# Kernel optimization log

Measured on AMD Instinct MI355X. Metric: run time of the kernel, lower is better.

Reference implementation:

```python
import jax, jax.numpy as jnp
import numpy as np

# ---- static configuration (from init_kwargs) ----
NY = NX = 256          # velocity model size
PML = 20               # PML width (cells) on every edge
FD_PAD = 2             # halo for 4th-order (accuracy=4) stencil
PAD = PML + FD_PAD
NYP = NY + 2 * PAD     # padded grid = 300
NXP = NX + 2 * PAD
DY = DX = 5.0          # grid spacing (m)
DT = 5e-4              # time step (s), CFL-stable for vmax=4000
NT = 250
NSHOT, NSRC, NREC = 2, 8, 64
PML_FREQ = 25.0
MAX_VEL = 4000.0

# 4th-order central FD coefficients
C1 = (1.0 / 12.0, -2.0 / 3.0, 0.0, 2.0 / 3.0, -1.0 / 12.0)   # d/dx
C2 = (-1.0 / 12.0, 4.0 / 3.0, -5.0 / 2.0, 4.0 / 3.0, -1.0 / 12.0)  # d2/dx2


def _fd(x, coefs, axis, h):
    """Central finite difference along `axis` with zero (Dirichlet) boundaries."""
    pad = [(0, 0)] * x.ndim
    pad[axis] = (2, 2)
    xp = jnp.pad(x, pad)
    n = x.shape[axis]
    out = None
    for i, c in enumerate(coefs):
        if c == 0.0:
            continue
        t = c * jax.lax.slice_in_dim(xp, i, i + n, axis=axis)
        out = t if out is None else out + t
    return out / h


def _pml_profiles(n, dx):
    """C-PML a/b profiles (Pasalic & McGarry 2010) along one padded axis."""
    i = jnp.arange(n, dtype=jnp.float32)
    lo = float(PAD)          # first interior cell
    hi = float(n - PAD - 1)  # last interior cell
    frac = jnp.clip(jnp.maximum(lo - i, i - hi) / PML, 0.0, 1.0)
    sigma_max = 3.0 * MAX_VEL * float(np.log(1000.0)) / (2.0 * PML * dx)
    sigma = sigma_max * frac ** 2
    alpha = float(np.pi) * PML_FREQ * (1.0 - frac)
    b = jnp.exp(-(sigma + alpha) * DT)
    a = sigma / (sigma + alpha + 1e-9) * (b - 1.0)
    return a.astype(jnp.float32), b.astype(jnp.float32)


def setup_inputs() -> dict:
    key = jax.random.key(0)
    k1, k2, k3, k4 = jax.random.split(key, 4)
    # realistic acoustic velocities 1500-4000 m/s
    v = 1500.0 + 2500.0 * jax.random.uniform(k1, (NY, NX), dtype=jnp.float32)
    source_amplitudes = jax.random.normal(k2, (NSHOT, NSRC, NT), dtype=jnp.float32)
    source_locations = jax.random.randint(k3, (NSHOT, NSRC, 2), 0, NY, dtype=jnp.int64)
    receiver_locations = jax.random.randint(k4, (NSHOT, NREC, 2), 0, NY, dtype=jnp.int64)
    return {
        "v": v,
        "source_amplitudes": source_amplitudes,
        "source_locations": source_locations,
        "receiver_locations": receiver_locations,
    }


def reference(v, source_amplitudes, source_locations, receiver_locations):
    # pad velocity into PML + fd halo by edge replication (per docstring)
    vp = jnp.pad(v, PAD, mode="edge")
    v2dt2 = (vp * vp) * (DT * DT)  # [NYP, NXP]

    ay, by = _pml_profiles(NYP, DY)
    ay, by = ay[:, None], by[:, None]   # broadcast over x
    ax, bx = _pml_profiles(NXP, DX)      # broadcast over y

    sy = source_locations[..., 0] + PAD   # [NSHOT, NSRC]
    sx = source_locations[..., 1] + PAD
    ry = receiver_locations[..., 0] + PAD  # [NSHOT, NREC]
    rx = receiver_locations[..., 1] + PAD
    shot_s = jnp.arange(NSHOT)[:, None]
    src_scale = v2dt2[sy, sx]  # source term is scaled by v^2*dt^2

    zeros = jnp.zeros((NSHOT, NYP, NXP), jnp.float32)
    carry0 = (zeros, zeros, zeros, zeros, zeros, zeros)

    def step(carry, amp_t):
        wfc, wfm, psiy, psix, zetay, zetax = carry
        # y direction
        dwdy = _fd(wfc, C1, -2, DY)
        d2wdy2 = _fd(wfc, C2, -2, DY * DY)
        psiy = by * psiy + ay * dwdy
        dpsiydy = _fd(psiy, C1, -2, DY)
        zetay = by * zetay + ay * (d2wdy2 + dpsiydy)
        # x direction
        dwdx = _fd(wfc, C1, -1, DX)
        d2wdx2 = _fd(wfc, C2, -1, DX * DX)
        psix = bx * psix + ax * dwdx
        dpsixdx = _fd(psix, C1, -1, DX)
        zetax = bx * zetax + ax * (d2wdx2 + dpsixdx)
        # leapfrog time update with C-PML corrections
        lap = d2wdy2 + d2wdx2 + dpsiydy + dpsixdx + zetay + zetax
        wfp = 2.0 * wfc - wfm + v2dt2 * lap
        wfp = wfp.at[shot_s, sy, sx].add(src_scale * amp_t)
        rec = wfp[shot_s, ry, rx]  # [NSHOT, NREC]
        return (wfp, wfc, psiy, psix, zetay, zetax), rec

    amps = jnp.moveaxis(source_amplitudes, -1, 0)  # [NT, NSHOT, NSRC]
    _, recs = jax.lax.scan(step, carry0, amps)
    return jnp.moveaxis(recs, 0, -1)  # [NSHOT, NREC, NT]
```

## Files before the change

kernel.cpp:

```cpp
#include <hip/hip_runtime.h>
#include <cstdint>

#define NYD   256
#define NXD   256
#define PADC  22
#define NYP_  300
#define NXP_  300
#define NTT   250
#define NSHOT_ 2
#define NSRC_  8
#define NREC_  64
#define DT_   0.0005f

#define GDN   28
#define STP   356
#define FP    (STP*STP)

#define NTX   5
#define NTY   75
#define TPS   375
#define NWG   750

__global__ void zero_kernel(float* __restrict__ p, long n) {
    long i = (long)blockIdx.x * blockDim.x + threadIdx.x;
    long stride = (long)gridDim.x * blockDim.x;
    for (; i < n; i += stride) p[i] = 0.0f;
}

__global__ void populate_kernel(const float* __restrict__ v,
                                const int* __restrict__ srcloc,
                                const int* __restrict__ recloc,
                                float* __restrict__ v2dt2,
                                float* __restrict__ prof,
                                unsigned* __restrict__ srcbin,
                                unsigned long long* __restrict__ recbin) {
    int i = blockIdx.x * 256 + threadIdx.x;

    if (i < NYP_ * NXP_) {
        int y = i / NXP_, x = i % NXP_;
        int vy = min(max(y - PADC, 0), NYD - 1);
        int vx = min(max(x - PADC, 0), NXD - 1);
        float vv = v[vy * NXD + vx];
        v2dt2[(y + GDN) * STP + (x + GDN)] = vv * vv * (DT_ * DT_);
    }

    if (i < NYP_) {
        float fi = (float)i;
        float d = fmaxf(22.0f - fi, fi - 277.0f);
        float frac = fminf(fmaxf(d * (1.0f / 20.0f), 0.0f), 1.0f);
        float sigma_max = 3.0f * 4000.0f * logf(1000.0f) / (2.0f * 20.0f * 5.0f);
        float sigma = sigma_max * frac * frac;
        float alpha = 3.14159265358979323846f * 25.0f * (1.0f - frac);
        float b = expf(-(sigma + alpha) * DT_);
        float a = sigma / (sigma + alpha + 1e-9f) * (b - 1.0f);
        prof[GDN + i] = a;
        prof[STP + GDN + i] = b;
    }

    if (i < NSHOT_ * NSRC_) {
        int sy = srcloc[2 * i] + PADC;
        int sx = srcloc[2 * i + 1] + PADC;
        int shot = i / NSRC_;
        int tl = (sy / 4) * NTX + (sx / 64);
        atomicOr(&srcbin[shot * TPS + tl], 1u << (i % NSRC_));
    }

    if (i >= 1024 && i < 1024 + NSHOT_ * NREC_) {
        int j = i - 1024;
        int ry = recloc[2 * j] + PADC;
        int rx = recloc[2 * j + 1] + PADC;
        int shot = j / NREC_;
        int tl = (ry / 4) * NTX + (rx / 64);
        atomicOr(&recbin[shot * TPS + tl], 1ull << (j % NREC_));
    }
}

__global__ __launch_bounds__(256) void step_kernel(
    const float* __restrict__ wfc_g,
    float* __restrict__ wfn_g,
    const float* __restrict__ pyr_g, float* __restrict__ pyw_g,
    const float* __restrict__ pxr_g, float* __restrict__ pxw_g,
    float* __restrict__ zy_g, float* __restrict__ zx_g,
    const float* __restrict__ v2_g, const float* __restrict__ prof,
    const unsigned* __restrict__ srcbin,
    const unsigned long long* __restrict__ recbin,
    const int* __restrict__ srcloc, const int* __restrict__ recloc,
    const float* __restrict__ amps,
    float* __restrict__ out,
    int t) {
    int orig = blockIdx.x;
    int xcd = orig & 7, idx = orig >> 3;
    int wgid = (xcd < 6) ? xcd * 94 + idx : 6 * 94 + (xcd - 6) * 93 + idx;
    int shot = wgid / TPS;
    int tl   = wgid - shot * TPS;
    int ty0  = (tl / NTX) * 4;
    int tx0  = (tl % NTX) * 64;

    const float* wfc = wfc_g + shot * FP;
    float*       wfn = wfn_g + shot * FP;
    const float* pyr = pyr_g + shot * FP;
    float*       pyw = pyw_g + shot * FP;
    const float* pxr = pxr_g + shot * FP;
    float*       pxw = pxw_g + shot * FP;
    float*       zyg = zy_g  + shot * FP;
    float*       zxg = zx_g  + shot * FP;

    __shared__ float swf[12][72];
    __shared__ float spy[8][64];
    __shared__ float spx[4][72];
    __shared__ float sya[8], syb[8], sxa[68], sxb[68];
    __shared__ int   ssy[NSRC_], ssx[NSRC_], sry[NREC_], srx[NREC_];
    __shared__ unsigned sbs;
    __shared__ unsigned long long sbr;

    const int tid = threadIdx.x;
    const int lx = tid & 63, ly = tid >> 6;
    const int y = ty0 + ly, x = tx0 + lx;
    const int g = (y + GDN) * STP + (x + GDN);

    float wm = wfn[g];
    float zy = zyg[g];
    float zx = zxg[g];
    float vd = v2_g[g];

    if (tid < 216) {
        int rr = tid / 18, cc = tid % 18;
        const float4 val = *(reinterpret_cast<const float4*>(
            wfc + (ty0 - 4 + rr + GDN) * STP + (tx0 - 4 + GDN)) + cc);
        *reinterpret_cast<float4*>(&swf[rr][cc * 4]) = val;
    }
    if (tid < 128) {
        int rr = tid / 16, cc = tid % 16;
        const float4 val = *(reinterpret_cast<const float4*>(
            pyr + (ty0 - 2 + rr + GDN) * STP + (tx0 + GDN)) + cc);
        *reinterpret_cast<float4*>(&spy[rr][cc * 4]) = val;
    }
    if (tid < 72) {
        int rr = tid / 18, cc = tid % 18;
        const float4 val = *(reinterpret_cast<const float4*>(
            pxr + (ty0 + rr + GDN) * STP + (tx0 - 4 + GDN)) + cc);
        *reinterpret_cast<float4*>(&spx[rr][cc * 4]) = val;
    }
    if (tid < 8) {
        sya[tid] = prof[GDN + ty0 - 2 + tid];
        syb[tid] = prof[STP + GDN + ty0 - 2 + tid];
        ssy[tid] = srcloc[(shot * NSRC_ + tid) * 2]     + PADC;
        ssx[tid] = srcloc[(shot * NSRC_ + tid) * 2 + 1] + PADC;
    }
    if (tid < 68) {
        sxa[tid] = prof[GDN + tx0 - 2 + tid];
        sxb[tid] = prof[STP + GDN + tx0 - 2 + tid];
    }
    if (tid < NREC_) {
        sry[tid] = recloc[(shot * NREC_ + tid) * 2]     + PADC;
        srx[tid] = recloc[(shot * NREC_ + tid) * 2 + 1] + PADC;
    }
    if (tid == 0) {
        sbs = srcbin[shot * TPS + tl];
        sbr = recbin[shot * TPS + tl];
    }
    __syncthreads();

    const float ih  = 0.2f;
    const float ih2 = 0.04f;
    const float C1A = 2.0f / 3.0f, C1B = 1.0f / 12.0f;
    const float C2A = 4.0f / 3.0f, C2B = -1.0f / 12.0f, C2C = -2.5f;

    float wy[9];
#pragma unroll
    for (int k = 0; k < 9; k++) wy[k] = swf[ly + k][lx + 4];
    float wx[9];
#pragma unroll
    for (int k = 0; k < 9; k++) wx[k] = (k == 4) ? wy[4] : swf[ly + 4][lx + k];

    float d2y = (C2B * (wy[2] + wy[6]) + C2A * (wy[3] + wy[5]) + C2C * wy[4]) * ih2;
    float d2x = (C2B * (wx[2] + wx[6]) + C2A * (wx[3] + wx[5]) + C2C * wx[4]) * ih2;

    float pny[5], pnx[5];
#pragma unroll
    for (int j = 0; j < 5; j++) {
        float dwdy = (C1A * (wy[j + 3] - wy[j + 1]) - C1B * (wy[j + 4] - wy[j])) * ih;
        pny[j] = syb[ly + j] * spy[ly + j][lx] + sya[ly + j] * dwdy;
        float dwdx = (C1A * (wx[j + 3] - wx[j + 1]) - C1B * (wx[j + 4] - wx[j])) * ih;
        pnx[j] = sxb[lx + j] * spx[ly][lx + j + 2] + sxa[lx + j] * dwdx;
    }

    float dpsiy = (C1A * (pny[3] - pny[1]) - C1B * (pny[4] - pny[0])) * ih;
    float dpsix = (C1A * (pnx[3] - pnx[1]) - C1B * (pnx[4] - pnx[0])) * ih;

    float ay_ = sya[ly + 2], by_ = syb[ly + 2];
    float ax_ = sxa[lx + 2], bx_ = sxb[lx + 2];

    zy = by_ * zy + ay_ * (d2y + dpsiy);
    zx = bx_ * zx + ax_ * (d2x + dpsix);

    float lap = d2y + d2x + dpsiy + dpsix + zy + zx;
    float wfp = 2.0f * wy[4] - wm + vd * lap;

    if (sbs) {
#pragma unroll
        for (int q = 0; q < NSRC_; q++)
            if ((sbs & (1u << q)) && ssy[q] == y && ssx[q] == x)
                wfp += vd * amps[(shot * NSRC_ + q) * NTT + t];
    }

    wfn[g] = wfp;
    pyw[g] = pny[2];
    pxw[g] = pnx[2];
    zyg[g] = zy;
    zxg[g] = zx;

    unsigned long long rb = sbr;
    while (rb) {
        int r = __ffsll(rb) - 1;
        rb &= rb - 1;
        if (sry[r] == y && srx[r] == x)
            out[(shot * NREC_ + r) * NTT + t] = wfp;
    }
}

extern "C" void kernel_launch(void* const* d_in, const int* in_sizes, int n_in,
                              void* d_out, int out_size, void* d_ws, size_t ws_size,
                              hipStream_t stream) {
    const float* v      = (const float*)d_in[0];
    const float* amps   = (const float*)d_in[1];
    const int*   srcloc = (const int*)d_in[2];
    const int*   recloc = (const int*)d_in[3];
    float* out = (float*)d_out;

    float* base = (float*)d_ws;
    float* WF0 = base;
    float* WF1 = WF0 + 2L * FP;
    float* PY0 = WF1 + 2L * FP;
    float* PY1 = PY0 + 2L * FP;
    float* PX0 = PY1 + 2L * FP;
    float* PX1 = PX0 + 2L * FP;
    float* ZY  = PX1 + 2L * FP;
    float* ZX  = ZY  + 2L * FP;
    float* V2  = ZX  + 2L * FP;
    float* PROF = V2 + FP;
    unsigned* SRCBIN = (unsigned*)(PROF + 2 * STP);
    unsigned long long* RECBIN = (unsigned long long*)(SRCBIN + NSHOT_ * TPS);

    const long total_words = 17L * FP + 2 * STP + NSHOT_ * TPS + 2L * NSHOT_ * TPS;

    zero_kernel<<<2048, 256, 0, stream>>>(base, total_words);
    populate_kernel<<<(NYP_ * NXP_ + 255) / 256, 256, 0, stream>>>(
        v, srcloc, recloc, V2, PROF, SRCBIN, RECBIN);

    for (int t = 0; t < NTT; t++) {
        const bool o = (t & 1);
        step_kernel<<<NWG, 256, 0, stream>>>(
            o ? WF1 : WF0, o ? WF0 : WF1,
            o ? PY1 : PY0, o ? PY0 : PY1,
            o ? PX1 : PX0, o ? PX0 : PX1,
            ZY, ZX, V2, PROF, SRCBIN, RECBIN,
            srcloc, recloc, amps, out, t);
    }
}
```

Measured before the change: 1.275 ms.

## Fuse two timesteps per launch with halo-expanded tiles in shared memory

Replaces the single-step kernel with a temporal-blocking kernel that advances two leapfrog steps per launch. It loads 8x32 tiles with wide halos into LDS, computes the intermediate wavefield, psi and zeta over an extended region, then finishes the second step for the interior. This halves the number of launches and the global memory round trips of wavefield and PML state. The cost is redundant halo computation, more LDS, extra ping-pong buffers, and brute-force source checks in place of source binning.

```diff
diff --git a/kernel.cpp b/kernel.cpp
--- a/kernel.cpp
+++ b/kernel.cpp
@@ -16,10 +16,12 @@
 #define STP   356
 #define FP    (STP*STP)
 
-#define NTX   5
-#define NTY   75
-#define TPS   375
-#define NWG   750
+#define BY    8
+#define BX    32
+#define NTX   10
+#define NTY   38
+#define TPS   380
+#define NWG   760
 
 __global__ void zero_kernel(float* __restrict__ p, long n) {
     long i = (long)blockIdx.x * blockDim.x + threadIdx.x;
@@ -28,11 +30,9 @@
 }
 
 __global__ void populate_kernel(const float* __restrict__ v,
-                                const int* __restrict__ srcloc,
                                 const int* __restrict__ recloc,
                                 float* __restrict__ v2dt2,
                                 float* __restrict__ prof,
-                                unsigned* __restrict__ srcbin,
                                 unsigned long long* __restrict__ recbin) {
     int i = blockIdx.x * 256 + threadIdx.x;
 
@@ -57,108 +57,114 @@
         prof[STP + GDN + i] = b;
     }
 
-    if (i < NSHOT_ * NSRC_) {
-        int sy = srcloc[2 * i] + PADC;
-        int sx = srcloc[2 * i + 1] + PADC;
-        int shot = i / NSRC_;
-        int tl = (sy / 4) * NTX + (sx / 64);
-        atomicOr(&srcbin[shot * TPS + tl], 1u << (i % NSRC_));
-    }
-
-    if (i >= 1024 && i < 1024 + NSHOT_ * NREC_) {
-        int j = i - 1024;
-        int ry = recloc[2 * j] + PADC;
-        int rx = recloc[2 * j + 1] + PADC;
-        int shot = j / NREC_;
-        int tl = (ry / 4) * NTX + (rx / 64);
-        atomicOr(&recbin[shot * TPS + tl], 1ull << (j % NREC_));
+    if (i < NSHOT_ * NREC_) {
+        int ry = recloc[2 * i] + PADC;
+        int rx = recloc[2 * i + 1] + PADC;
+        int shot = i / NREC_;
+        int tl = (ry / BY) * NTX + (rx / BX);
+        atomicOr(&recbin[shot * TPS + tl], 1ull << (i % NREC_));
     }
 }
 
-__global__ __launch_bounds__(256) void step_kernel(
+__global__ __launch_bounds__(256) void fused2_kernel(
+    const float* __restrict__ wfm_g,
     const float* __restrict__ wfc_g,
-    float* __restrict__ wfn_g,
+    float* __restrict__ w1_g,
+    float* __restrict__ w2_g,
     const float* __restrict__ pyr_g, float* __restrict__ pyw_g,
     const float* __restrict__ pxr_g, float* __restrict__ pxw_g,
-    float* __restrict__ zy_g, float* __restrict__ zx_g,
+    const float* __restrict__ zyr_g, float* __restrict__ zyw_g,
+    const float* __restrict__ zxr_g, float* __restrict__ zxw_g,
     const float* __restrict__ v2_g, const float* __restrict__ prof,
-    const unsigned* __restrict__ srcbin,
     const unsigned long long* __restrict__ recbin,
     const int* __restrict__ srcloc, const int* __restrict__ recloc,
     const float* __restrict__ amps,
     float* __restrict__ out,
     int t) {
-    int orig = blockIdx.x;
-    int xcd = orig & 7, idx = orig >> 3;
-    int wgid = (xcd < 6) ? xcd * 94 + idx : 6 * 94 + (xcd - 6) * 93 + idx;
-    int shot = wgid / TPS;
-    int tl   = wgid - shot * TPS;
-    int ty0  = (tl / NTX) * 4;
-    int tx0  = (tl % NTX) * 64;
-
+    const int orig = blockIdx.x;
+    const int wgid = (orig & 7) * 95 + (orig >> 3);
+    const int shot = wgid / TPS;
+    const int tl   = wgid - shot * TPS;
+    const int ty0  = (tl / NTX) * BY;
+    const int tx0  = (tl % NTX) * BX;
+
+    const float* wfm = wfm_g + shot * FP;
     const float* wfc = wfc_g + shot * FP;
-    float*       wfn = wfn_g + shot * FP;
+    float*       w1o = w1_g  + shot * FP;
+    float*       w2o = w2_g  + shot * FP;
     const float* pyr = pyr_g + shot * FP;
     float*       pyw = pyw_g + shot * FP;
     const float* pxr = pxr_g + shot * FP;
     float*       pxw = pxw_g + shot * FP;
-    float*       zyg = zy_g  + shot * FP;
-    float*       zxg = zx_g  + shot * FP;
-
-    __shared__ float swf[12][72];
-    __shared__ float spy[8][64];
-    __shared__ float spx[4][72];
-    __shared__ float sya[8], syb[8], sxa[68], sxb[68];
+    const float* zyr = zyr_g + shot * FP;
+    float*       zyw = zyw_g + shot * FP;
+    const float* zxr = zxr_g + shot * FP;
+    float*       zxw = zxw_g + shot * FP;
+
+    __shared__ float swf0[24][48];
+    __shared__ float spy [20][40];
+    __shared__ float spx [16][48];
+    __shared__ float swf1[16][40];
+    __shared__ float szy [16][40];
+    __shared__ float szx [16][40];
+    __shared__ float sv2 [16][40];
+    __shared__ float swm [16][40];
+    __shared__ float sya[24], syb[24], sxa[48], sxb[48];
     __shared__ int   ssy[NSRC_], ssx[NSRC_], sry[NREC_], srx[NREC_];
-    __shared__ unsigned sbs;
-    __shared__ unsigned long long sbr;
+    __shared__ unsigned long long srb;
 
     const int tid = threadIdx.x;
-    const int lx = tid & 63, ly = tid >> 6;
-    const int y = ty0 + ly, x = tx0 + lx;
-    const int g = (y + GDN) * STP + (x + GDN);
-
-    float wm = wfn[g];
-    float zy = zyg[g];
-    float zx = zxg[g];
-    float vd = v2_g[g];
-
-    if (tid < 216) {
-        int rr = tid / 18, cc = tid % 18;
-        const float4 val = *(reinterpret_cast<const float4*>(
-            wfc + (ty0 - 4 + rr + GDN) * STP + (tx0 - 4 + GDN)) + cc);
-        *reinterpret_cast<float4*>(&swf[rr][cc * 4]) = val;
-    }
-    if (tid < 128) {
-        int rr = tid / 16, cc = tid % 16;
-        const float4 val = *(reinterpret_cast<const float4*>(
-            pyr + (ty0 - 2 + rr + GDN) * STP + (tx0 + GDN)) + cc);
-        *reinterpret_cast<float4*>(&spy[rr][cc * 4]) = val;
-    }
-    if (tid < 72) {
-        int rr = tid / 18, cc = tid % 18;
-        const float4 val = *(reinterpret_cast<const float4*>(
-            pxr + (ty0 + rr + GDN) * STP + (tx0 - 4 + GDN)) + cc);
-        *reinterpret_cast<float4*>(&spx[rr][cc * 4]) = val;
-    }
-    if (tid < 8) {
-        sya[tid] = prof[GDN + ty0 - 2 + tid];
-        syb[tid] = prof[STP + GDN + ty0 - 2 + tid];
+
+#pragma unroll
+    for (int li = 0; li < 6; li++) {
+        int lin = tid + li * 256;
+        if (lin < 288) {
+            int rr = lin / 12, cc = lin % 12;
+            *reinterpret_cast<float4*>(&swf0[rr][cc * 4]) =
+                *reinterpret_cast<const float4*>(wfc + (ty0 - 8 + rr + GDN) * STP + (tx0 - 8 + GDN) + cc * 4);
+        } else if (lin < 488) {
+            int l = lin - 288; int rr = l / 10, cc = l % 10;
+            *reinterpret_cast<float4*>(&spy[rr][cc * 4]) =
+                *reinterpret_cast<const float4*>(pyr + (ty0 - 6 + rr + GDN) * STP + (tx0 - 4 + GDN) + cc * 4);
+        } else if (lin < 680) {
+            int l = lin - 488; int rr = l / 12, cc = l % 12;
+            *reinterpret_cast<float4*>(&spx[rr][cc * 4]) =
+                *reinterpret_cast<const float4*>(pxr + (ty0 - 4 + rr + GDN) * STP + (tx0 - 8 + GDN) + cc * 4);
+        } else if (lin < 840) {
+            int l = lin - 680; int rr = l / 10, cc = l % 10;
+            *reinterpret_cast<float4*>(&szy[rr][cc * 4]) =
+                *reinterpret_cast<const float4*>(zyr + (ty0 - 4 + rr + GDN) * STP + (tx0 - 4 + GDN) + cc * 4);
+        } else if (lin < 1000) {
+            int l = lin - 840; int rr = l / 10, cc = l % 10;
+            *reinterpret_cast<float4*>(&szx[rr][cc * 4]) =
+                *reinterpret_cast<const float4*>(zxr + (ty0 - 4 + rr + GDN) * STP + (tx0 - 4 + GDN) + cc * 4);
+        } else if (lin < 1160) {
+            int l = lin - 1000; int rr = l / 10, cc = l % 10;
+            *reinterpret_cast<float4*>(&sv2[rr][cc * 4]) =
+                *reinterpret_cast<const float4*>(v2_g + (ty0 - 4 + rr + GDN) * STP + (tx0 - 4 + GDN) + cc * 4);
+        } else if (lin < 1320) {
+            int l = lin - 1160; int rr = l / 10, cc = l % 10;
+            *reinterpret_cast<float4*>(&swm[rr][cc * 4]) =
+                *reinterpret_cast<const float4*>(wfm + (ty0 - 4 + rr + GDN) * STP + (tx0 - 4 + GDN) + cc * 4);
+        }
+    }
+    if (tid < 24) {
+        sya[tid] = prof[GDN + ty0 - 8 + tid];
+        syb[tid] = prof[STP + GDN + ty0 - 8 + tid];
+    }
+    if (tid < 48) {
+        sxa[tid] = prof[GDN + tx0 - 8 + tid];
+        sxb[tid] = prof[STP + GDN + tx0 - 8 + tid];
+    }
+    if (tid < NSRC_) {
         ssy[tid] = srcloc[(shot * NSRC_ + tid) * 2]     + PADC;
         ssx[tid] = srcloc[(shot * NSRC_ + tid) * 2 + 1] + PADC;
-    }
-    if (tid < 68) {
-        sxa[tid] = prof[GDN + tx0 - 2 + tid];
-        sxb[tid] = prof[STP + GDN + tx0 - 2 + tid];
     }
     if (tid < NREC_) {
         sry[tid] = recloc[(shot * NREC_ + tid) * 2]     + PADC;
         srx[tid] = recloc[(shot * NREC_ + tid) * 2 + 1] + PADC;
     }
-    if (tid == 0) {
-        sbs = srcbin[shot * TPS + tl];
-        sbr = recbin[shot * TPS + tl];
-    }
+    if (tid == 0) srb = recbin[shot * TPS + tl];
     __syncthreads();
 
     const float ih  = 0.2f;
@@ -166,56 +172,110 @@
     const float C1A = 2.0f / 3.0f, C1B = 1.0f / 12.0f;
     const float C2A = 4.0f / 3.0f, C2B = -1.0f / 12.0f, C2C = -2.5f;
 
-    float wy[9];
-#pragma unroll
-    for (int k = 0; k < 9; k++) wy[k] = swf[ly + k][lx + 4];
-    float wx[9];
-#pragma unroll
-    for (int k = 0; k < 9; k++) wx[k] = (k == 4) ? wy[4] : swf[ly + 4][lx + k];
-
-    float d2y = (C2B * (wy[2] + wy[6]) + C2A * (wy[3] + wy[5]) + C2C * wy[4]) * ih2;
-    float d2x = (C2B * (wx[2] + wx[6]) + C2A * (wx[3] + wx[5]) + C2C * wx[4]) * ih2;
-
-    float pny[5], pnx[5];
-#pragma unroll
-    for (int j = 0; j < 5; j++) {
-        float dwdy = (C1A * (wy[j + 3] - wy[j + 1]) - C1B * (wy[j + 4] - wy[j])) * ih;
-        pny[j] = syb[ly + j] * spy[ly + j][lx] + sya[ly + j] * dwdy;
-        float dwdx = (C1A * (wx[j + 3] - wx[j + 1]) - C1B * (wx[j + 4] - wx[j])) * ih;
-        pnx[j] = sxb[lx + j] * spx[ly][lx + j + 2] + sxa[lx + j] * dwdx;
-    }
-
-    float dpsiy = (C1A * (pny[3] - pny[1]) - C1B * (pny[4] - pny[0])) * ih;
-    float dpsix = (C1A * (pnx[3] - pnx[1]) - C1B * (pnx[4] - pnx[0])) * ih;
-
-    float ay_ = sya[ly + 2], by_ = syb[ly + 2];
-    float ax_ = sxa[lx + 2], bx_ = sxb[lx + 2];
-
-    zy = by_ * zy + ay_ * (d2y + dpsiy);
-    zx = bx_ * zx + ax_ * (d2x + dpsix);
-
-    float lap = d2y + d2x + dpsiy + dpsix + zy + zx;
-    float wfp = 2.0f * wy[4] - wm + vd * lap;
-
-    if (sbs) {
+#pragma unroll
+    for (int li = 0; li < 6; li++) {
+        int lin = tid + li * 256;
+        if (lin < 800) {
+            int r = lin / 40, c = lin % 40;
+            float dw = (C1A * (swf0[r + 3][c + 4] - swf0[r + 1][c + 4])
+                      - C1B * (swf0[r + 4][c + 4] - swf0[r][c + 4])) * ih;
+            spy[r][c] = syb[r + 2] * spy[r][c] + sya[r + 2] * dw;
+        } else if (lin < 1504) {
+            int l = lin - 800; int r = l / 44, c = l % 44 + 2;
+            float dw = (C1A * (swf0[r + 4][c + 1] - swf0[r + 4][c - 1])
+                      - C1B * (swf0[r + 4][c + 2] - swf0[r + 4][c - 2])) * ih;
+            spx[r][c] = sxb[c] * spx[r][c] + sxa[c] * dw;
+        }
+    }
+    __syncthreads();
+
+#pragma unroll
+    for (int li = 0; li < 3; li++) {
+        int lin = tid + li * 256;
+        if (lin < 640) {
+            int r = lin / 40, c = lin % 40;
+            float wc = swf0[r + 4][c + 4];
+            float d2y = (C2B * (swf0[r + 2][c + 4] + swf0[r + 6][c + 4])
+                       + C2A * (swf0[r + 3][c + 4] + swf0[r + 5][c + 4]) + C2C * wc) * ih2;
+            float d2x = (C2B * (swf0[r + 4][c + 2] + swf0[r + 4][c + 6])
+                       + C2A * (swf0[r + 4][c + 3] + swf0[r + 4][c + 5]) + C2C * wc) * ih2;
+            float dpy = (C1A * (spy[r + 3][c] - spy[r + 1][c])
+                       - C1B * (spy[r + 4][c] - spy[r][c])) * ih;
+            float dpx = (C1A * (spx[r][c + 5] - spx[r][c + 3])
+                       - C1B * (spx[r][c + 6] - spx[r][c + 2])) * ih;
+            float zy1 = syb[r + 4] * szy[r][c] + sya[r + 4] * (d2y + dpy);
+            float zx1 = sxb[c + 4] * szx[r][c] + sxa[c + 4] * (d2x + dpx);
+            szy[r][c] = zy1;
+            szx[r][c] = zx1;
+            float vd = sv2[r][c];
+            float w1 = 2.0f * wc - swm[r][c] + vd * (d2y + d2x + dpy + dpx + zy1 + zx1);
+            int y = ty0 - 4 + r, x = tx0 - 4 + c;
+#pragma unroll
+            for (int q = 0; q < NSRC_; q++)
+                if (ssy[q] == y && ssx[q] == x)
+                    w1 += vd * amps[(shot * NSRC_ + q) * NTT + t];
+            swf1[r][c] = w1;
+        }
+    }
+    __syncthreads();
+
+#pragma unroll
+    for (int li = 0; li < 3; li++) {
+        int lin = tid + li * 256;
+        if (lin < 384) {
+            int r = lin / 32, c = lin % 32;
+            float dw1 = (C1A * (swf1[r + 3][c + 4] - swf1[r + 1][c + 4])
+                       - C1B * (swf1[r + 4][c + 4] - swf1[r][c + 4])) * ih;
+            spy[r + 4][c + 4] = syb[r + 6] * spy[r + 4][c + 4] + sya[r + 6] * dw1;
+        } else if (lin < 672) {
+            int l = lin - 384; int r = l / 36, c2 = l % 36;
+            float dw1 = (C1A * (swf1[r + 4][c2 + 3] - swf1[r + 4][c2 + 1])
+                       - C1B * (swf1[r + 4][c2 + 4] - swf1[r + 4][c2])) * ih;
+            spx[r + 4][c2 + 6] = sxb[c2 + 6] * spx[r + 4][c2 + 6] + sxa[c2 + 6] * dw1;
+        }
+    }
+    __syncthreads();
+
+    {
+        int ly = tid >> 5, lx = tid & 31;
+        int y = ty0 + ly, x = tx0 + lx;
+        float w1c = swf1[ly + 4][lx + 4];
+        float d2y1 = (C2B * (swf1[ly + 2][lx + 4] + swf1[ly + 6][lx + 4])
+                    + C2A * (swf1[ly + 3][lx + 4] + swf1[ly + 5][lx + 4]) + C2C * w1c) * ih2;
+        float d2x1 = (C2B * (swf1[ly + 4][lx + 2] + swf1[ly + 4][lx + 6])
+                    + C2A * (swf1[ly + 4][lx + 3] + swf1[ly + 4][lx + 5]) + C2C * w1c) * ih2;
+        float dpy2 = (C1A * (spy[ly + 7][lx + 4] - spy[ly + 5][lx + 4])
+                    - C1B * (spy[ly + 8][lx + 4] - spy[ly + 4][lx + 4])) * ih;
+        float dpx2 = (C1A * (spx[ly + 4][lx + 9] - spx[ly + 4][lx + 7])
+                    - C1B * (spx[ly + 4][lx + 10] - spx[ly + 4][lx + 6])) * ih;
+        float zy2 = syb[ly + 8] * szy[ly + 4][lx + 4] + sya[ly + 8] * (d2y1 + dpy2);
+        float zx2 = sxb[lx + 8] * szx[ly + 4][lx + 4] + sxa[lx + 8] * (d2x1 + dpx2);
+        float vd = sv2[ly + 4][lx + 4];
+        float w2 = 2.0f * w1c - swf0[ly + 8][lx + 8]
+                 + vd * (d2y1 + d2x1 + dpy2 + dpx2 + zy2 + zx2);
 #pragma unroll
         for (int q = 0; q < NSRC_; q++)
-            if ((sbs & (1u << q)) && ssy[q] == y && ssx[q] == x)
-                wfp += vd * amps[(shot * NSRC_ + q) * NTT + t];
-    }
-
-    wfn[g] = wfp;
-    pyw[g] = pny[2];
-    pxw[g] = pnx[2];
-    zyg[g] = zy;
-    zxg[g] = zx;
-
-    unsigned long long rb = sbr;
-    while (rb) {
-        int r = __ffsll(rb) - 1;
-        rb &= rb - 1;
-        if (sry[r] == y && srx[r] == x)
-            out[(shot * NREC_ + r) * NTT + t] = wfp;
+            if (ssy[q] == y && ssx[q] == x)
+                w2 += vd * amps[(shot * NSRC_ + q) * NTT + t + 1];
+
+        if (y < NYP_ && x < NXP_) {
+            int g = (y + GDN) * STP + (x + GDN);
+            w1o[g] = w1c;
+            w2o[g] = w2;
+            pyw[g] = spy[ly + 6][lx + 4];
+            pxw[g] = spx[ly + 4][lx + 8];
+            zyw[g] = zy2;
+            zxw[g] = zx2;
+            unsigned long long rb = srb;
+            while (rb) {
+                int r = __ffsll(rb) - 1;
+                rb &= rb - 1;
+                if (sry[r] == y && srx[r] == x) {
+                    out[(shot * NREC_ + r) * NTT + t]     = w1c;
+                    out[(shot * NREC_ + r) * NTT + t + 1] = w2;
+                }
+            }
+        }
     }
 }
 
@@ -229,32 +289,37 @@
     float* out = (float*)d_out;
 
     float* base = (float*)d_ws;
-    float* WF0 = base;
-    float* WF1 = WF0 + 2L * FP;
-    float* PY0 = WF1 + 2L * FP;
+    float* W0  = base;
+    float* W1  = W0  + 2L * FP;
+    float* W2  = W1  + 2L * FP;
+    float* W3  = W2  + 2L * FP;
+    float* PY0 = W3  + 2L * FP;
     float* PY1 = PY0 + 2L * FP;
     float* PX0 = PY1 + 2L * FP;
     float* PX1 = PX0 + 2L * FP;
-    float* ZY  = PX1 + 2L * FP;
-    float* ZX  = ZY  + 2L * FP;
-    float* V2  = ZX  + 2L * FP;
+    float* ZY0 = PX1 + 2L * FP;
+    float* ZY1 = ZY0 + 2L * FP;
+    float* ZX0 = ZY1 + 2L * FP;
+    float* ZX1 = ZX0 + 2L * FP;
+    float* V2  = ZX1 + 2L * FP;
     float* PROF = V2 + FP;
-    unsigned* SRCBIN = (unsigned*)(PROF + 2 * STP);
-    unsigned long long* RECBIN = (unsigned long long*)(SRCBIN + NSHOT_ * TPS);
-
-    const long total_words = 17L * FP + 2 * STP + NSHOT_ * TPS + 2L * NSHOT_ * TPS;
+    unsigned long long* RECBIN = (unsigned long long*)(PROF + 2 * STP);
+
+    const long total_words = 25L * FP + 2 * STP + 2L * NSHOT_ * TPS;
 
     zero_kernel<<<2048, 256, 0, stream>>>(base, total_words);
     populate_kernel<<<(NYP_ * NXP_ + 255) / 256, 256, 0, stream>>>(
-        v, srcloc, recloc, V2, PROF, SRCBIN, RECBIN);
-
-    for (int t = 0; t < NTT; t++) {
-        const bool o = (t & 1);
-        step_kernel<<<NWG, 256, 0, stream>>>(
-            o ? WF1 : WF0, o ? WF0 : WF1,
+        v, recloc, V2, PROF, RECBIN);
+
+    for (int k = 0; k < NTT / 2; k++) {
+        const bool o = (k & 1);
+        fused2_kernel<<<NWG, 256, 0, stream>>>(
+            o ? W2 : W0, o ? W3 : W1,
+            o ? W0 : W2, o ? W1 : W3,
             o ? PY1 : PY0, o ? PY0 : PY1,
             o ? PX1 : PX0, o ? PX0 : PX1,
-            ZY, ZX, V2, PROF, SRCBIN, RECBIN,
-            srcloc, recloc, amps, out, t);
+            o ? ZY1 : ZY0, o ? ZY0 : ZY1,
+            o ? ZX1 : ZX0, o ? ZX0 : ZX1,
+            V2, PROF, RECBIN, srcloc, recloc, amps, out, 2 * k);
     }
 }
```

Result: slower. 1.315 ms (+3.1%).

## Replace per-step kernel launches with persistent cooperative kernel using neighbor flags

Applied to the files above, without the earlier changes.

Launches one cooperative persistent kernel of 190 workgroups (512 threads, 16x64 tiles) that loops over all 250 time steps. Workgroups synchronise through per-tile progress counters, waiting only on their four neighbours, and the zeta and previous-wavefield state stays in registers across steps. This removes 250 kernel launches and the per-step reload of the zeta, wfm and velocity arrays. The cost is spin-wait overhead, reliance on agent-scope relaxed atomics for ordering, and fewer workgroups in flight. The old per-step path remains as a fallback if the cooperative launch fails.

```diff
diff --git a/kernel.cpp b/kernel.cpp
--- a/kernel.cpp
+++ b/kernel.cpp
@@ -17,9 +17,22 @@
 #define FP    (STP*STP)
 
 #define NTX   5
-#define NTY   75
 #define TPS   375
 #define NWG   750
+
+#define BY2   16
+#define NTY2  19
+#define TPS2  95
+#define NWG2  190
+
+__device__ __forceinline__ unsigned long long ld_agent_u64(const float* p) {
+    return __hip_atomic_load((const unsigned long long*)p,
+                             __ATOMIC_RELAXED, __HIP_MEMORY_SCOPE_AGENT);
+}
+__device__ __forceinline__ void st_agent_f32(float* p, float v) {
+    __hip_atomic_store((unsigned*)p, __float_as_uint(v),
+                       __ATOMIC_RELAXED, __HIP_MEMORY_SCOPE_AGENT);
+}
 
 __global__ void zero_kernel(float* __restrict__ p, long n) {
     long i = (long)blockIdx.x * blockDim.x + threadIdx.x;
@@ -32,8 +45,10 @@
                                 const int* __restrict__ recloc,
                                 float* __restrict__ v2dt2,
                                 float* __restrict__ prof,
-                                unsigned* __restrict__ srcbin,
-                                unsigned long long* __restrict__ recbin) {
+                                unsigned* __restrict__ srcb4,
+                                unsigned long long* __restrict__ recb4,
+                                unsigned* __restrict__ srcb16,
+                                unsigned long long* __restrict__ recb16) {
     int i = blockIdx.x * 256 + threadIdx.x;
 
     if (i < NYP_ * NXP_) {
@@ -61,8 +76,8 @@
         int sy = srcloc[2 * i] + PADC;
         int sx = srcloc[2 * i + 1] + PADC;
         int shot = i / NSRC_;
-        int tl = (sy / 4) * NTX + (sx / 64);
-        atomicOr(&srcbin[shot * TPS + tl], 1u << (i % NSRC_));
+        atomicOr(&srcb4[shot * TPS + (sy / 4) * NTX + (sx / 64)], 1u << (i % NSRC_));
+        atomicOr(&srcb16[shot * TPS2 + (sy / BY2) * 5 + (sx / 64)], 1u << (i % NSRC_));
     }
 
     if (i >= 1024 && i < 1024 + NSHOT_ * NREC_) {
@@ -70,14 +85,170 @@
         int ry = recloc[2 * j] + PADC;
         int rx = recloc[2 * j + 1] + PADC;
         int shot = j / NREC_;
-        int tl = (ry / 4) * NTX + (rx / 64);
-        atomicOr(&recbin[shot * TPS + tl], 1ull << (j % NREC_));
+        atomicOr(&recb4[shot * TPS + (ry / 4) * NTX + (rx / 64)], 1ull << (j % NREC_));
+        atomicOr(&recb16[shot * TPS2 + (ry / BY2) * 5 + (rx / 64)], 1ull << (j % NREC_));
+    }
+}
+
+__global__ __launch_bounds__(512) void persist_kernel(
+    float* wfA, float* wfB, float* pyA, float* pyB, float* pxA, float* pxB,
+    const float* __restrict__ v2g, const float* __restrict__ profg,
+    const unsigned* __restrict__ srcb, const unsigned long long* __restrict__ recb,
+    int* prog,
+    const int* __restrict__ srcloc, const int* __restrict__ recloc,
+    const float* __restrict__ amps,
+    float* __restrict__ out) {
+    const int me   = blockIdx.x;
+    const int shot = me / TPS2;
+    const int tl   = me - shot * TPS2;
+    const int tyt  = tl / 5, txt = tl % 5;
+    const int ty0  = tyt * BY2, tx0 = txt * 64;
+
+    const int nUp = (tyt > 0)        ? me - 5 : me;
+    const int nDn = (tyt < NTY2 - 1) ? me + 5 : me;
+    const int nL  = (txt > 0)        ? me - 1 : me;
+    const int nR  = (txt < 4)        ? me + 1 : me;
+
+    __shared__ alignas(8) float swf[24][72];
+    __shared__ alignas(8) float spy[20][64];
+    __shared__ alignas(8) float spx[16][72];
+    __shared__ float sya[20], syb[20], sxa[68], sxb[68];
+    __shared__ int   ssy[NSRC_], ssx[NSRC_], sry[NREC_], srx[NREC_];
+    __shared__ unsigned sbs;
+    __shared__ unsigned long long sbr;
+
+    const int tid = threadIdx.x;
+    const int lx = tid & 63, ly = tid >> 6;
+
+    if (tid < 20) {
+        sya[tid] = profg[GDN + ty0 - 2 + tid];
+        syb[tid] = profg[STP + GDN + ty0 - 2 + tid];
+    }
+    if (tid < 68) {
+        sxa[tid] = profg[GDN + tx0 - 2 + tid];
+        sxb[tid] = profg[STP + GDN + tx0 - 2 + tid];
+    }
+    if (tid < NSRC_) {
+        ssy[tid] = srcloc[(shot * NSRC_ + tid) * 2]     + PADC;
+        ssx[tid] = srcloc[(shot * NSRC_ + tid) * 2 + 1] + PADC;
+    }
+    if (tid < NREC_) {
+        sry[tid] = recloc[(shot * NREC_ + tid) * 2]     + PADC;
+        srx[tid] = recloc[(shot * NREC_ + tid) * 2 + 1] + PADC;
+    }
+    if (tid == 0) { sbs = srcb[shot * TPS2 + tl]; sbr = recb[shot * TPS2 + tl]; }
+
+    float zyr[2] = {0.f, 0.f}, zxr[2] = {0.f, 0.f}, wmr[2] = {0.f, 0.f}, vdr[2];
+#pragma unroll
+    for (int c = 0; c < 2; ++c)
+        vdr[c] = v2g[(ty0 + ly + 8 * c + GDN) * STP + (tx0 + lx + GDN)];
+
+    const float* wfr = wfA + shot * FP;  float* wfw = wfB + shot * FP;
+    const float* pyr = pyA + shot * FP;  float* pyw = pyB + shot * FP;
+    const float* pxr = pxA + shot * FP;  float* pxw = pxB + shot * FP;
+
+    __syncthreads();
+
+    const float ih  = 0.2f;
+    const float ih2 = 0.04f;
+    const float C1A = 2.0f / 3.0f, C1B = 1.0f / 12.0f;
+    const float C2A = 4.0f / 3.0f, C2B = -1.0f / 12.0f, C2C = -2.5f;
+
+#pragma unroll 1
+    for (int it = 0; it < NTT; ++it) {
+        if (tid < 4) {
+            const int nb = (tid == 0) ? nUp : (tid == 1) ? nDn : (tid == 2) ? nL : nR;
+            while (__hip_atomic_load(&prog[nb], __ATOMIC_RELAXED, __HIP_MEMORY_SCOPE_AGENT) < it)
+                __builtin_amdgcn_s_sleep(1);
+        }
+        __syncthreads();
+
+#pragma unroll
+        for (int li = 0; li < 5; ++li) {
+            int lin = tid + li * 512;
+            if (lin < 864) {
+                int rr = lin / 36, cc = lin % 36;
+                *(unsigned long long*)&swf[rr][cc * 2] =
+                    ld_agent_u64(wfr + (ty0 - 4 + rr + GDN) * STP + (tx0 - 4 + GDN) + cc * 2);
+            } else if (lin < 1504) {
+                int l = lin - 864, rr = l / 32, cc = l % 32;
+                *(unsigned long long*)&spy[rr][cc * 2] =
+                    ld_agent_u64(pyr + (ty0 - 2 + rr + GDN) * STP + (tx0 + GDN) + cc * 2);
+            } else if (lin < 2080) {
+                int l = lin - 1504, rr = l / 36, cc = l % 36;
+                *(unsigned long long*)&spx[rr][cc * 2] =
+                    ld_agent_u64(pxr + (ty0 + rr + GDN) * STP + (tx0 - 4 + GDN) + cc * 2);
+            }
+        }
+        __syncthreads();
+
+#pragma unroll
+        for (int c = 0; c < 2; ++c) {
+            const int yy = ly + 8 * c;
+            const int y = ty0 + yy, x = tx0 + lx;
+
+            float wy[9], wx[9];
+#pragma unroll
+            for (int k = 0; k < 9; ++k) wy[k] = swf[yy + k][lx + 4];
+#pragma unroll
+            for (int k = 0; k < 9; ++k) wx[k] = (k == 4) ? wy[4] : swf[yy + 4][lx + k];
+
+            float d2y = (C2B * (wy[2] + wy[6]) + C2A * (wy[3] + wy[5]) + C2C * wy[4]) * ih2;
+            float d2x = (C2B * (wx[2] + wx[6]) + C2A * (wx[3] + wx[5]) + C2C * wx[4]) * ih2;
+
+            float pny[5], pnx[5];
+#pragma unroll
+            for (int j = 0; j < 5; ++j) {
+                float dwdy = (C1A * (wy[j + 3] - wy[j + 1]) - C1B * (wy[j + 4] - wy[j])) * ih;
+                pny[j] = syb[yy + j] * spy[yy + j][lx] + sya[yy + j] * dwdy;
+                float dwdx = (C1A * (wx[j + 3] - wx[j + 1]) - C1B * (wx[j + 4] - wx[j])) * ih;
+                pnx[j] = sxb[lx + j] * spx[yy][lx + j + 2] + sxa[lx + j] * dwdx;
+            }
+            float dpsiy = (C1A * (pny[3] - pny[1]) - C1B * (pny[4] - pny[0])) * ih;
+            float dpsix = (C1A * (pnx[3] - pnx[1]) - C1B * (pnx[4] - pnx[0])) * ih;
+
+            float zyn = syb[yy + 2] * zyr[c] + sya[yy + 2] * (d2y + dpsiy);
+            float zxn = sxb[lx + 2] * zxr[c] + sxa[lx + 2] * (d2x + dpsix);
+            zyr[c] = zyn; zxr[c] = zxn;
+
+            float lap = d2y + d2x + dpsiy + dpsix + zyn + zxn;
+            float wfp = 2.0f * wy[4] - wmr[c] + vdr[c] * lap;
+
+            if (sbs) {
+#pragma unroll
+                for (int q = 0; q < NSRC_; ++q)
+                    if ((sbs & (1u << q)) && ssy[q] == y && ssx[q] == x)
+                        wfp += vdr[c] * amps[(shot * NSRC_ + q) * NTT + it];
+            }
+            wmr[c] = wy[4];
+
+            const int g = (y + GDN) * STP + (x + GDN);
+            st_agent_f32(wfw + g, wfp);
+            st_agent_f32(pyw + g, pny[2]);
+            st_agent_f32(pxw + g, pnx[2]);
+
+            unsigned long long rb = sbr;
+            while (rb) {
+                int r = __ffsll(rb) - 1;
+                rb &= rb - 1;
+                if (sry[r] == y && srx[r] == x)
+                    out[(shot * NREC_ + r) * NTT + it] = wfp;
+            }
+        }
+
+        asm volatile("s_waitcnt vmcnt(0)" ::: "memory");
+        __syncthreads();
+        if (tid == 0)
+            __hip_atomic_store(&prog[me], it + 1, __ATOMIC_RELAXED, __HIP_MEMORY_SCOPE_AGENT);
+
+        const float* t0 = wfr; wfr = wfw; wfw = (float*)t0;
+        const float* t1 = pyr; pyr = pyw; pyw = (float*)t1;
+        const float* t2 = pxr; pxr = pxw; pxw = (float*)t2;
     }
 }
 
 __global__ __launch_bounds__(256) void step_kernel(
-    const float* __restrict__ wfc_g,
-    float* __restrict__ wfn_g,
+    const float* __restrict__ wfc_g, float* __restrict__ wfn_g,
     const float* __restrict__ pyr_g, float* __restrict__ pyw_g,
     const float* __restrict__ pxr_g, float* __restrict__ pxw_g,
     float* __restrict__ zy_g, float* __restrict__ zx_g,
@@ -85,9 +256,7 @@
     const unsigned* __restrict__ srcbin,
     const unsigned long long* __restrict__ recbin,
     const int* __restrict__ srcloc, const int* __restrict__ recloc,
-    const float* __restrict__ amps,
-    float* __restrict__ out,
-    int t) {
+    const float* __restrict__ amps, float* __restrict__ out, int t) {
     int orig = blockIdx.x;
     int xcd = orig & 7, idx = orig >> 3;
     int wgid = (xcd < 6) ? xcd * 94 + idx : 6 * 94 + (xcd - 6) * 93 + idx;
@@ -125,21 +294,18 @@
 
     if (tid < 216) {
         int rr = tid / 18, cc = tid % 18;
-        const float4 val = *(reinterpret_cast<const float4*>(
-            wfc + (ty0 - 4 + rr + GDN) * STP + (tx0 - 4 + GDN)) + cc);
-        *reinterpret_cast<float4*>(&swf[rr][cc * 4]) = val;
+        *reinterpret_cast<float4*>(&swf[rr][cc * 4]) =
+            *(reinterpret_cast<const float4*>(wfc + (ty0 - 4 + rr + GDN) * STP + (tx0 - 4 + GDN)) + cc);
     }
     if (tid < 128) {
         int rr = tid / 16, cc = tid % 16;
-        const float4 val = *(reinterpret_cast<const float4*>(
-            pyr + (ty0 - 2 + rr + GDN) * STP + (tx0 + GDN)) + cc);
-        *reinterpret_cast<float4*>(&spy[rr][cc * 4]) = val;
+        *reinterpret_cast<float4*>(&spy[rr][cc * 4]) =
+            *(reinterpret_cast<const float4*>(pyr + (ty0 - 2 + rr + GDN) * STP + (tx0 + GDN)) + cc);
     }
     if (tid < 72) {
         int rr = tid / 18, cc = tid % 18;
-        const float4 val = *(reinterpret_cast<const float4*>(
-            pxr + (ty0 + rr + GDN) * STP + (tx0 - 4 + GDN)) + cc);
-        *reinterpret_cast<float4*>(&spx[rr][cc * 4]) = val;
+        *reinterpret_cast<float4*>(&spx[rr][cc * 4]) =
+            *(reinterpret_cast<const float4*>(pxr + (ty0 + rr + GDN) * STP + (tx0 - 4 + GDN)) + cc);
     }
     if (tid < 8) {
         sya[tid] = prof[GDN + ty0 - 2 + tid];
@@ -155,14 +321,10 @@
         sry[tid] = recloc[(shot * NREC_ + tid) * 2]     + PADC;
         srx[tid] = recloc[(shot * NREC_ + tid) * 2 + 1] + PADC;
     }
-    if (tid == 0) {
-        sbs = srcbin[shot * TPS + tl];
-        sbr = recbin[shot * TPS + tl];
-    }
+    if (tid == 0) { sbs = srcbin[shot * TPS + tl]; sbr = recbin[shot * TPS + tl]; }
     __syncthreads();
 
-    const float ih  = 0.2f;
-    const float ih2 = 0.04f;
+    const float ih = 0.2f, ih2 = 0.04f;
     const float C1A = 2.0f / 3.0f, C1B = 1.0f / 12.0f;
     const float C2A = 4.0f / 3.0f, C2B = -1.0f / 12.0f, C2C = -2.5f;
 
@@ -239,22 +401,38 @@
     float* ZX  = ZY  + 2L * FP;
     float* V2  = ZX  + 2L * FP;
     float* PROF = V2 + FP;
-    unsigned* SRCBIN = (unsigned*)(PROF + 2 * STP);
-    unsigned long long* RECBIN = (unsigned long long*)(SRCBIN + NSHOT_ * TPS);
-
-    const long total_words = 17L * FP + 2 * STP + NSHOT_ * TPS + 2L * NSHOT_ * TPS;
+    unsigned long long* RECB4  = (unsigned long long*)(PROF + 2 * STP);
+    unsigned long long* RECB16 = RECB4 + NSHOT_ * TPS;
+    unsigned* SRCB4  = (unsigned*)(RECB16 + NSHOT_ * TPS2);
+    unsigned* SRCB16 = SRCB4 + NSHOT_ * TPS;
+    int*      PROG   = (int*)(SRCB16 + NSHOT_ * TPS2);
+
+    const long total_words = 17L * FP + 2 * STP
+                           + 2L * NSHOT_ * TPS + 2L * NSHOT_ * TPS2
+                           + NSHOT_ * TPS + NSHOT_ * TPS2
+                           + NWG2;
 
     zero_kernel<<<2048, 256, 0, stream>>>(base, total_words);
     populate_kernel<<<(NYP_ * NXP_ + 255) / 256, 256, 0, stream>>>(
-        v, srcloc, recloc, V2, PROF, SRCBIN, RECBIN);
-
-    for (int t = 0; t < NTT; t++) {
-        const bool o = (t & 1);
-        step_kernel<<<NWG, 256, 0, stream>>>(
-            o ? WF1 : WF0, o ? WF0 : WF1,
-            o ? PY1 : PY0, o ? PY0 : PY1,
-            o ? PX1 : PX0, o ? PX0 : PX1,
-            ZY, ZX, V2, PROF, SRCBIN, RECBIN,
-            srcloc, recloc, amps, out, t);
-    }
-}
+        v, srcloc, recloc, V2, PROF, SRCB4, RECB4, SRCB16, RECB16);
+
+    void* args[] = {
+        (void*)&WF0, (void*)&WF1, (void*)&PY0, (void*)&PY1, (void*)&PX0, (void*)&PX1,
+        (void*)&V2, (void*)&PROF, (void*)&SRCB16, (void*)&RECB16, (void*)&PROG,
+        (void*)&srcloc, (void*)&recloc, (void*)&amps, (void*)&out
+    };
+    hipError_t e = hipLaunchCooperativeKernel((void*)persist_kernel,
+                                              dim3(NWG2), dim3(512), args, 0, stream);
+
+    if (e != hipSuccess) {
+        for (int t = 0; t < NTT; t++) {
+            const bool o = (t & 1);
+            step_kernel<<<NWG, 256, 0, stream>>>(
+                o ? WF1 : WF0, o ? WF0 : WF1,
+                o ? PY1 : PY0, o ? PY0 : PY1,
+                o ? PX1 : PX0, o ? PX0 : PX1,
+                ZY, ZX, V2, PROF, SRCB4, RECB4,
+                srcloc, recloc, amps, out, t);
+        }
+    }
+}
```

After: 1.520 ms. 19.2% more time.
